# Kernel tuning notes

Hardware: AMD Instinct MI355X
Metric: run time of the kernel (lower is better)

## Reference

```python
import jax, jax.numpy as jnp
import numpy as np

ANGLE_SCALE = 100.0
DIST_SCALE = 100.0
DIST_BOUNDARY = 0.0
HID = 128
N_HIDDEN = 2  # output_layer
EPS = 1e-08


def _mlp(x, w0, b0, ws, bs):
    # Linear, then N_HIDDEN x (ReLU, Linear)
    h = x @ w0 + b0
    for i in range(ws.shape[0]):
        h = jax.nn.relu(h) @ ws[i] + bs[i]
    return h


def _capsule_endpoints(x):
    # x: [..., 9] -> A, B endpoints of capsule segment, radius r
    c, s = jnp.cos(x[..., 3:4] * ANGLE_SCALE), jnp.sin(x[..., 3:4] * ANGLE_SCALE)
    half = x[..., 2:3] / 2
    ctr = x[..., 0:2]
    off = jnp.concatenate([half * c, half * s], axis=-1)
    return ctr - off, ctr + off, x[..., 4:5]


def _pt_seg_dist(P, A, AB, AB_sq):
    t = jnp.clip(((P - A) * AB).sum(-1, keepdims=True) / AB_sq, 0.0, 1.0)
    Q = A + t * AB
    return jnp.linalg.norm(P - Q, axis=-1, keepdims=True)


def _dist_to_capsule(init_e, query_e):
    A1, B1, r1 = _capsule_endpoints(init_e)
    A2, B2, r2 = _capsule_endpoints(query_e)
    A1B1, A2B2 = B1 - A1, B2 - A2
    s1 = (A1B1 ** 2).sum(-1, keepdims=True) + EPS
    s2 = (A2B2 ** 2).sum(-1, keepdims=True) + EPS
    d = jnp.minimum(
        jnp.minimum(_pt_seg_dist(A2, A1, A1B1, s1), _pt_seg_dist(B2, A1, A1B1, s1)),
        jnp.minimum(_pt_seg_dist(A1, A2, A2B2, s2), _pt_seg_dist(B1, A2, A2B2, s2)),
    )
    return d - r1 - r2


def setup_inputs() -> dict:
    key = jax.random.key(0)
    ks = jax.random.split(key, 32)
    B, O, T = 64, 64, 64
    f = lambda k, shp, scale=1.0: jax.random.normal(k, shp, dtype=jnp.float32) * scale
    inp = {
        'init_x': f(ks[0], (B, O, 9)),
        'query_x': f(ks[1], (B, T, 9)),
        'init_v': f(ks[2], (B, O, 2)),
        'query_v': f(ks[3], (B, T, 2)),
        'init_angular_v': f(ks[4], (B, O, 1)),
        'query_angular_v': f(ks[5], (B, T, 1)),
        'trunk_w0': f(ks[6], (9, HID), 0.3), 'trunk_b0': f(ks[7], (HID,), 0.1),
        'trunk_ws': f(ks[8], (N_HIDDEN, HID, HID), 0.08), 'trunk_bs': f(ks[9], (N_HIDDEN, HID), 0.1),
        'branch_w0': f(ks[10], (5, HID), 0.3), 'branch_b0': f(ks[11], (HID,), 0.1),
        'branch_ws': f(ks[12], (N_HIDDEN, HID, HID), 0.08), 'branch_bs': f(ks[13], (N_HIDDEN, HID), 0.1),
        'out_w': f(ks[14], (HID, 3), 0.08), 'out_b': f(ks[15], (3,), 0.1),
        'spring_w0': f(ks[16], (1, HID), 0.3), 'spring_b0': f(ks[17], (HID,), 0.1),
        'spring_w1': f(ks[18], (HID, 1), 0.08), 'spring_b1': f(ks[19], (1,), 0.1),
        'joint_w0': f(ks[20], (15, HID), 0.3), 'joint_b0': f(ks[21], (HID,), 0.1),
        'joint_w1': f(ks[22], (HID, 2), 0.08), 'joint_b1': f(ks[23], (2,), 0.1),
    }
    return inp


def reference(init_x, query_x, init_v, query_v, init_angular_v, query_angular_v,
              trunk_w0, trunk_b0, trunk_ws, trunk_bs,
              branch_w0, branch_b0, branch_ws, branch_bs,
              out_w, out_b, spring_w0, spring_b0, spring_w1, spring_b1,
              joint_w0, joint_b0, joint_w1, joint_b1):
    B, O, _ = init_x.shape
    T = query_x.shape[1]
    # pairwise broadcast: init along obj axis (dim1), query along target axis (dim2)
    init_e = jnp.broadcast_to(init_x[:, :, None, :], (B, O, T, 9))
    query_e = jnp.broadcast_to(query_x[:, None, :, :], (B, O, T, 9))
    rel = query_e[..., :2] - init_e[..., :2]
    query_e = jnp.concatenate([rel, query_e[..., 2:]], axis=-1)
    init_e = jnp.concatenate([jnp.zeros_like(rel), init_e[..., 2:]], axis=-1)
    qv = query_v[:, None, :, :] - init_v[:, :, None, :]           # [B,O,T,2]
    qav = query_angular_v[:, None, :, :] - init_angular_v[:, :, None, :]  # [B,O,T,1]
    iav = jnp.broadcast_to(init_angular_v[:, :, None, :], (B, O, T, 1))

    dist = _dist_to_capsule(init_e, query_e)
    dist_mask = (dist <= DIST_BOUNDARY).astype(jnp.float32)
    dist_input = dist * dist_mask * DIST_SCALE

    branch_in = init_e[..., :5]
    trunk_in = jnp.concatenate([query_e[..., :5], qv, qav, dist_input], axis=-1)
    branch_out = _mlp(branch_in, branch_w0, branch_b0, branch_ws, branch_bs)
    trunk_out = _mlp(trunk_in, trunk_w0, trunk_b0, trunk_ws, trunk_bs)
    force = (branch_out * trunk_out) @ out_w + out_b  # [B,O,T,3]

    # spring force
    have_spring = ((init_e[..., 8:9] == query_e[..., 8:9]) & (init_e[..., 8:9] > 0)).astype(jnp.float32)
    dvec = init_e[..., :2] - query_e[..., :2]
    length = jnp.linalg.norm(dvec, axis=-1, keepdims=True)
    dvec = dvec / (length + EPS)
    sf = jax.nn.relu(length @ spring_w0 + spring_b0) @ spring_w1 + spring_b1  # [B,O,T,1]
    sf = sf * dvec
    sf = jnp.concatenate([sf, jnp.zeros_like(sf[..., :1])], axis=-1) * have_spring

    # joint force (torch .long() truncates toward zero)
    i7, q7 = init_e[..., 7:8], query_e[..., 7:8]
    have_joint = ((jnp.trunc(i7) == jnp.trunc(q7)) & (i7 > 0)).astype(jnp.float32)
    joint_in = jnp.concatenate([init_e[..., :5], query_e[..., :5], qv, iav, qav, i7 - jnp.trunc(i7)], axis=-1)
    jf = jax.nn.relu(joint_in @ joint_w0 + joint_b0) @ joint_w1 + joint_b1  # [B,O,T,2]
    jf = jf * have_joint
    jf = jnp.concatenate([jf, jnp.zeros_like(jf[..., :1])], axis=-1)

    force = force * dist_mask + sf + jf
    return force
```

## Files before the change

### kernel.cpp

```cpp
#include <hip/hip_runtime.h>
#include <math.h>


typedef _Float16 h4v __attribute__((ext_vector_type(4)));
typedef _Float16 h8v __attribute__((ext_vector_type(8)));
typedef float    f4v __attribute__((ext_vector_type(4)));

#define AH 136

#define TW0_OFF 0
#define JW0_OFF 4096
#define TWS_OFF 8192
#define BW0_OFF 40960
#define BWS_OFF 45056
#define W_TOTAL 77824
#define BR_OFF_F (W_TOTAL/2)

#define H_ACTA 0
#define H_ACTB 8704
#define H_TINB 8704
#define H_JINB 10752
#define SMH_SIZE 17408

#define F_SCAL  0
#define SMF_SIZE 384

#define FRAG_BLOCKS 304
#define BR_BLOCKS   256

__global__ __launch_bounds__(256)
void prep_kernel(const float* __restrict__ tw0, const float* __restrict__ tws,
                 const float* __restrict__ jw0, const float* __restrict__ bw0,
                 const float* __restrict__ bws, const float* __restrict__ bb0,
                 const float* __restrict__ bbs, const float* __restrict__ init_x,
                 _Float16* __restrict__ wsH, float* __restrict__ brw)
{
    __shared__ float bsm[2*16*132];
    const int tid = threadIdx.x;

    if (blockIdx.x < FRAG_BLOCKS) {
        int idx = blockIdx.x * 256 + tid;
        if (idx >= W_TOTAL) return;
        const int j = idx & 7;
        const int lane = (idx >> 3) & 63;
        const int q = lane >> 4, r = lane & 15;
        _Float16 v;
        if (idx < JW0_OFF) {
            int mt = idx >> 9;
            int k = q*8 + j, m = mt*16 + r;
            v = (k < 9) ? (_Float16)tw0[k*128 + m] : (_Float16)0.f;
        } else if (idx < TWS_OFF) {
            int mt = (idx - JW0_OFF) >> 9;
            int k = q*8 + j, m = mt*16 + r;
            v = (k < 15) ? (_Float16)jw0[k*128 + m] : (_Float16)0.f;
        } else if (idx < BW0_OFF) {
            int e = idx - TWS_OFF;
            int ks = (e >> 9) & 3, mt = (e >> 11) & 7, l = e >> 14;
            int k = ks*32 + q*8 + j, m = mt*16 + r;
            v = (_Float16)tws[l*16384 + k*128 + m];
        } else if (idx < BWS_OFF) {
            int mt = (idx - BW0_OFF) >> 9;
            int k = q*8 + j, m = mt*16 + r;
            v = (k < 5) ? (_Float16)bw0[k*128 + m] : (_Float16)0.f;
        } else {
            int e = idx - BWS_OFF;
            int ks = (e >> 9) & 3, mt = (e >> 11) & 7, l = e >> 14;
            int k = ks*32 + q*8 + j, m = mt*16 + r;
            v = (_Float16)bws[l*16384 + k*128 + m];
        }
        wsH[idx] = v;
        return;
    }

    const int blk2 = blockIdx.x - FRAG_BLOCKS;
    const int row0 = blk2*16;
    const int lane = tid & 63, w = tid >> 6;
    const int q = lane >> 4, r = lane & 15;
    float* h0 = bsm;
    float* h1 = bsm + 16*132;

    for (int e = tid; e < 2048; e += 256) {
        const int rw = e >> 7, n = e & 127;
        const float* ixp = init_x + (row0 + rw)*9;
        float acc = bb0[n];
        acc = fmaf(ixp[2], bw0[2*128 + n], acc);
        acc = fmaf(ixp[3], bw0[3*128 + n], acc);
        acc = fmaf(ixp[4], bw0[4*128 + n], acc);
        h0[rw*132 + n] = acc;
    }
    __syncthreads();

    #pragma unroll
    for (int L = 0; L < 2; ++L) {
        const float* Wg = bws + L*16384;
        const float* bi = bbs + L*128;
        const float* in = (L == 0) ? h0 : h1;
        #pragma unroll
        for (int mi = 0; mi < 2; ++mi) {
            const int mt = w + mi*4;
            const int m0 = mt*16 + q*4;
            h8v af[4];
            #pragma unroll
            for (int ks = 0; ks < 4; ++ks)
                #pragma unroll
                for (int j = 0; j < 8; ++j)
                    af[ks][j] = (_Float16)Wg[(ks*32 + q*8 + j)*128 + mt*16 + r];
            f4v acc = *(const f4v*)&bi[m0];
            #pragma unroll
            for (int ks = 0; ks < 4; ++ks) {
                f4v x0 = *(const f4v*)&in[r*132 + ks*32 + q*8];
                f4v x1 = *(const f4v*)&in[r*132 + ks*32 + q*8 + 4];
                h8v bf;
                #pragma unroll
                for (int i = 0; i < 4; ++i) {
                    bf[i]   = (_Float16)fmaxf(x0[i], 0.f);
                    bf[4+i] = (_Float16)fmaxf(x1[i], 0.f);
                }
                acc = __builtin_amdgcn_mfma_f32_16x16x32_f16(af[ks], bf, acc, 0, 0, 0);
            }
            if (L == 0)
                *(f4v*)&h1[r*132 + m0] = acc;
            else
                *(f4v*)&brw[(row0 + r)*128 + m0] = acc;
        }
        __syncthreads();
    }
}

__device__ __forceinline__ void layerK32_rw(const h8v af[2],
        const float* __restrict__ bias, const _Float16* __restrict__ inB,
        _Float16* __restrict__ actOut, int lane, int w)
{
    const int q = lane >> 4, r = lane & 15;
    #pragma unroll
    for (int nt = 0; nt < 4; ++nt) {
        h8v bf = *(const h8v*)&inB[(nt*64 + lane)*8];
        #pragma unroll
        for (int mi = 0; mi < 2; ++mi) {
            f4v acc = *(const f4v*)&bias[(2*w + mi)*16 + q*4];
            acc = __builtin_amdgcn_mfma_f32_16x16x32_f16(af[mi], bf, acc, 0, 0, 0);
            h4v o;
            #pragma unroll
            for (int i = 0; i < 4; ++i) o[i] = (_Float16)fmaxf(acc[i], 0.f);
            *(h4v*)&actOut[(nt*16 + r)*AH + (2*w + mi)*16 + q*4] = o;
        }
    }
}

__device__ __forceinline__ void layerK128_rw(const h8v af[2][4],
        const float* __restrict__ bias, const _Float16* __restrict__ actIn,
        _Float16* __restrict__ actOut, int lane, int w)
{
    const int q = lane >> 4, r = lane & 15;
    #pragma unroll
    for (int nt = 0; nt < 4; ++nt) {
        h8v bf[4];
        #pragma unroll
        for (int ks = 0; ks < 4; ++ks)
            bf[ks] = *(const h8v*)&actIn[(nt*16 + r)*AH + ks*32 + q*8];
        #pragma unroll
        for (int mi = 0; mi < 2; ++mi) {
            f4v acc = *(const f4v*)&bias[(2*w + mi)*16 + q*4];
            #pragma unroll
            for (int ks = 0; ks < 4; ++ks)
                acc = __builtin_amdgcn_mfma_f32_16x16x32_f16(af[mi][ks], bf[ks], acc, 0, 0, 0);
            h4v o;
            #pragma unroll
            for (int i = 0; i < 4; ++i) o[i] = (_Float16)fmaxf(acc[i], 0.f);
            *(h4v*)&actOut[(nt*16 + r)*AH + (2*w + mi)*16 + q*4] = o;
        }
    }
}

__device__ __forceinline__ void layerK128_regs_rw(const h8v af[2][4],
        const float* __restrict__ bias, const _Float16* __restrict__ actIn,
        f4v accT[2][4], int lane, int w)
{
    const int q = lane >> 4, r = lane & 15;
    #pragma unroll
    for (int nt = 0; nt < 4; ++nt) {
        h8v bf[4];
        #pragma unroll
        for (int ks = 0; ks < 4; ++ks)
            bf[ks] = *(const h8v*)&actIn[(nt*16 + r)*AH + ks*32 + q*8];
        #pragma unroll
        for (int mi = 0; mi < 2; ++mi) {
            f4v acc = *(const f4v*)&bias[(2*w + mi)*16 + q*4];
            #pragma unroll
            for (int ks = 0; ks < 4; ++ks)
                acc = __builtin_amdgcn_mfma_f32_16x16x32_f16(af[mi][ks], bf[ks], acc, 0, 0, 0);
            accT[mi][nt] = acc;
        }
    }
}

__global__ __launch_bounds__(256, 3)
void ff_kernel(const float* __restrict__ init_x,  const float* __restrict__ query_x,
               const float* __restrict__ init_v,  const float* __restrict__ query_v,
               const float* __restrict__ init_av, const float* __restrict__ query_av,
               const float* __restrict__ tb0, const float* __restrict__ tbs,
               const float* __restrict__ out_w, const float* __restrict__ out_b,
               const float* __restrict__ sw0, const float* __restrict__ sb0,
               const float* __restrict__ sw1, const float* __restrict__ sb1,
               const float* __restrict__ jb0,
               const float* __restrict__ jw1, const float* __restrict__ jb1,
               const _Float16* __restrict__ wsH, const float* __restrict__ brw,
               float* __restrict__ out)
{
    __shared__ __align__(16) _Float16 smh[SMH_SIZE];
    __shared__ float smf[SMF_SIZE];
    float* const fred = (float*)smh;
    const int tid = threadIdx.x;
    const int bid = blockIdx.x;
    const int o  = bid & 63;
    const int b  = bid >> 6;
    const int lane = tid & 63, w = tid >> 6;
    const int q = lane >> 4, r = lane & 15;
    const float* ix = init_x + (b*64 + o)*9;

    h8v afT0[2], afJ0[2], afT1[2][4], afT2[2][4];
    f4v br[2];
    #pragma unroll
    for (int mi = 0; mi < 2; ++mi) {
        const int mtg = 2*w + mi;
        afT0[mi] = *(const h8v*)&wsH[TW0_OFF + (mtg*64 + lane)*8];
        afJ0[mi] = *(const h8v*)&wsH[JW0_OFF + (mtg*64 + lane)*8];
        #pragma unroll
        for (int ks = 0; ks < 4; ++ks) {
            afT1[mi][ks] = *(const h8v*)&wsH[TWS_OFF + ((mtg*4 + ks)*64 + lane)*8];
            afT2[mi][ks] = *(const h8v*)&wsH[TWS_OFF + 16384 + ((mtg*4 + ks)*64 + lane)*8];
        }
        br[mi] = *(const f4v*)&brw[bid*128 + mtg*16 + q*4];
    }

    {
        const int tq = w*16 + r;
        const float* qx = query_x + (b*64 + tq)*9;
        const float ix0 = ix[0], ix1 = ix[1], ix2 = ix[2], ix3 = ix[3], ix4 = ix[4];
        const float ix7 = ix[7], ix8 = ix[8];
        const float qx0 = qx[0], qx1 = qx[1], qx2 = qx[2], qx3 = qx[3], qx4 = qx[4];
        const float qx7 = qx[7], qx8 = qx[8];
        const float rel0 = qx0 - ix0, rel1 = qx1 - ix1;

        float s1v, c1v; sincosf(ix3 * 100.f, &s1v, &c1v);
        float s2v, c2v; sincosf(qx3 * 100.f, &s2v, &c2v);
        const float h1 = ix2 * 0.5f, h2 = qx2 * 0.5f;
        const float o1x = h1*c1v, o1y = h1*s1v;
        const float o2x = h2*c2v, o2y = h2*s2v;
        const float A1x = -o1x, A1y = -o1y;
        const float A2x = rel0 - o2x, A2y = rel1 - o2y;
        const float B2x = rel0 + o2x, B2y = rel1 + o2y;
        const float ab1x = 2.f*o1x, ab1y = 2.f*o1y;
        const float ab2x = 2.f*o2x, ab2y = 2.f*o2y;
        const float s1sq = ab1x*ab1x + ab1y*ab1y + 1e-8f;
        const float s2sq = ab2x*ab2x + ab2y*ab2y + 1e-8f;

        float Px, Py, Ax, Ay, ABx, ABy, ss;
        if (q < 2) {
            Ax = A1x; Ay = A1y; ABx = ab1x; ABy = ab1y; ss = s1sq;
            Px = (q == 0) ? A2x : B2x;  Py = (q == 0) ? A2y : B2y;
        } else {
            Ax = A2x; Ay = A2y; ABx = ab2x; ABy = ab2y; ss = s2sq;
            Px = (q == 2) ? A1x : o1x;  Py = (q == 2) ? A1y : o1y;
        }
        float t = ((Px - Ax)*ABx + (Py - Ay)*ABy) / ss;
        t = fminf(fmaxf(t, 0.f), 1.f);
        const float dx = Px - (Ax + t*ABx);
        const float dy = Py - (Ay + t*ABy);
        float dq = sqrtf(dx*dx + dy*dy);
        dq = fminf(dq, __shfl_xor(dq, 16));
        dq = fminf(dq, __shfl_xor(dq, 32));

        if (q == 0) {
            const float dist = dq - ix4 - qx4;
            const float mask = (dist <= 0.f) ? 1.f : 0.f;
            const float dinp = dist * mask * 100.f;
            const float qv0 = query_v[(b*64+tq)*2+0] - init_v[(b*64+o)*2+0];
            const float qv1 = query_v[(b*64+tq)*2+1] - init_v[(b*64+o)*2+1];
            const float iav = init_av[b*64+o];
            const float qav = query_av[b*64+tq] - iav;

            const int fb = w*512 + r*8;
            h8v t0, t1 = {}, z = {};
            t0[0]=(_Float16)rel0; t0[1]=(_Float16)rel1; t0[2]=(_Float16)qx2;
            t0[3]=(_Float16)qx3;  t0[4]=(_Float16)qx4;  t0[5]=(_Float16)qv0;
            t0[6]=(_Float16)qv1;  t0[7]=(_Float16)qav;
            t1[0]=(_Float16)dinp;
            *(h8v*)&smh[H_TINB + fb]       = t0;
            *(h8v*)&smh[H_TINB + fb + 128] = t1;
            *(h8v*)&smh[H_TINB + fb + 256] = z;
            *(h8v*)&smh[H_TINB + fb + 384] = z;
            h8v j0, j1 = {};
            j0[0]=(_Float16)0.f;  j0[1]=(_Float16)0.f;  j0[2]=(_Float16)ix2;
            j0[3]=(_Float16)ix3;  j0[4]=(_Float16)ix4;  j0[5]=(_Float16)rel0;
            j0[6]=(_Float16)rel1; j0[7]=(_Float16)qx2;
            j1[0]=(_Float16)qx3;  j1[1]=(_Float16)qx4;  j1[2]=(_Float16)qv0;
            j1[3]=(_Float16)qv1;  j1[4]=(_Float16)iav;  j1[5]=(_Float16)qav;
            j1[6]=(_Float16)(ix7 - truncf(ix7));
            *(h8v*)&smh[H_JINB + fb]       = j0;
            *(h8v*)&smh[H_JINB + fb + 128] = j1;
            *(h8v*)&smh[H_JINB + fb + 256] = z;
            *(h8v*)&smh[H_JINB + fb + 384] = z;

            const float len = sqrtf(rel0*rel0 + rel1*rel1);
            const float inv = 1.f / (len + 1e-8f);
            smf[F_SCAL +       tq] = mask;
            smf[F_SCAL +  64 + tq] = len;
            smf[F_SCAL + 128 + tq] = -rel0 * inv;
            smf[F_SCAL + 192 + tq] = -rel1 * inv;
            smf[F_SCAL + 256 + tq] = ((ix8 == qx8) && (ix8 > 0.f)) ? 1.f : 0.f;
            smf[F_SCAL + 320 + tq] = ((truncf(ix7) == truncf(qx7)) && (ix7 > 0.f)) ? 1.f : 0.f;
        }
    }
    __syncthreads();

    float jf0[4] = {0,0,0,0}, jf1[4] = {0,0,0,0};
    layerK32_rw(afT0, tb0, smh + H_TINB, smh + H_ACTA, lane, w);
    {
        f4v bv[2], jwa[2], jwb[2];
        #pragma unroll
        for (int mi = 0; mi < 2; ++mi) {
            const int m0 = (2*w + mi)*16 + q*4;
            bv[mi]  = *(const f4v*)&jb0[m0];
            jwa[mi] = *(const f4v*)&jw1[m0*2];
            jwb[mi] = *(const f4v*)&jw1[m0*2 + 4];
        }
        #pragma unroll
        for (int nt = 0; nt < 4; ++nt) {
            h8v bf = *(const h8v*)&smh[H_JINB + (nt*64 + lane)*8];
            #pragma unroll
            for (int mi = 0; mi < 2; ++mi) {
                f4v a = bv[mi];
                a = __builtin_amdgcn_mfma_f32_16x16x32_f16(afJ0[mi], bf, a, 0, 0, 0);
                float jw[8] = {jwa[mi][0], jwa[mi][1], jwa[mi][2], jwa[mi][3],
                               jwb[mi][0], jwb[mi][1], jwb[mi][2], jwb[mi][3]};
                #pragma unroll
                for (int i = 0; i < 4; ++i) {
                    const float jh = fmaxf(a[i], 0.f);
                    jf0[nt] = fmaf(jh, jw[i*2+0], jf0[nt]);
                    jf1[nt] = fmaf(jh, jw[i*2+1], jf1[nt]);
                }
            }
        }
    }
    __syncthreads();

    layerK128_rw(afT1, tbs, smh + H_ACTA, smh + H_ACTB, lane, w);
    __syncthreads();

    f4v accT[2][4];
    layerK128_regs_rw(afT2, tbs + 128, smh + H_ACTB, accT, lane, w);

    float f0[4] = {0,0,0,0}, f1[4] = {0,0,0,0}, f2[4] = {0,0,0,0};
    float sp[4] = {0,0,0,0};

    #pragma unroll
    for (int mi = 0; mi < 2; ++mi) {
        const int m0 = (2*w + mi)*16 + q*4;
        f4v oa = *(const f4v*)&out_w[m0*3];
        f4v ob = *(const f4v*)&out_w[m0*3 + 4];
        f4v oc = *(const f4v*)&out_w[m0*3 + 8];
        float ow[12] = {oa[0],oa[1],oa[2],oa[3], ob[0],ob[1],ob[2],ob[3],
                        oc[0],oc[1],oc[2],oc[3]};
        #pragma unroll
        for (int nt = 0; nt < 4; ++nt)
            #pragma unroll
            for (int i = 0; i < 4; ++i) {
                const float prod = accT[mi][nt][i] * br[mi][i];
                f0[nt] = fmaf(prod, ow[i*3+0], f0[nt]);
                f1[nt] = fmaf(prod, ow[i*3+1], f1[nt]);
                f2[nt] = fmaf(prod, ow[i*3+2], f2[nt]);
            }
    }
    {
        float lenv[4];
        #pragma unroll
        for (int nt = 0; nt < 4; ++nt) lenv[nt] = smf[F_SCAL + 64 + nt*16 + r];
        #pragma unroll
        for (int mi = 0; mi < 2; ++mi) {
            const int m0 = (2*w + mi)*16 + q*4;
            f4v w0 = *(const f4v*)&sw0[m0];
            f4v b0 = *(const f4v*)&sb0[m0];
            f4v w1 = *(const f4v*)&sw1[m0];
            #pragma unroll
            for (int i = 0; i < 4; ++i)
                #pragma unroll
                for (int nt = 0; nt < 4; ++nt) {
                    const float sv = fmaxf(fmaf(lenv[nt], w0[i], b0[i]), 0.f);
                    sp[nt] = fmaf(sv, w1[i], sp[nt]);
                }
        }
    }
    #pragma unroll
    for (int nt = 0; nt < 4; ++nt) {
        float v[6] = {f0[nt], f1[nt], f2[nt], jf0[nt], jf1[nt], sp[nt]};
        #pragma unroll
        for (int k = 0; k < 6; ++k) {
            v[k] += __shfl_xor(v[k], 16);
            v[k] += __shfl_xor(v[k], 32);
        }
        if (lane < 16) {
            float* rd = &fred[((nt*16 + r)*4 + w)*7];
            rd[0]=v[0]; rd[1]=v[1]; rd[2]=v[2]; rd[3]=v[3]; rd[4]=v[4]; rd[5]=v[5];
        }
    }
    __syncthreads();

    if (tid < 64) {
        const int t = tid;
        float s0=0.f, s1=0.f, s2=0.f, s3=0.f, s4=0.f, s5=0.f;
        #pragma unroll
        for (int ww = 0; ww < 4; ++ww) {
            const float* rd = &fred[(t*4 + ww)*7];
            s0 += rd[0]; s1 += rd[1]; s2 += rd[2];
            s3 += rd[3]; s4 += rd[4]; s5 += rd[5];
        }
        const float mask = smf[F_SCAL + t];
        const float dvx  = smf[F_SCAL + 128 + t];
        const float dvy  = smf[F_SCAL + 192 + t];
        const float hs   = smf[F_SCAL + 256 + t];
        const float hj   = smf[F_SCAL + 320 + t];
        const float sf = (s5 + sb1[0]) * hs;
        const float j0 = (s3 + jb1[0]) * hj;
        const float j1 = (s4 + jb1[1]) * hj;
        float* op = out + (((b*64 + o)*64) + t)*3;
        op[0] = (s0 + out_b[0])*mask + sf*dvx + j0;
        op[1] = (s1 + out_b[1])*mask + sf*dvy + j1;
        op[2] = (s2 + out_b[2])*mask;
    }
}

extern "C" void kernel_launch(void* const* d_in, const int* in_sizes, int n_in,
                              void* d_out, int out_size, void* d_ws, size_t ws_size,
                              hipStream_t stream) {
    (void)in_sizes; (void)n_in; (void)out_size; (void)ws_size;
    _Float16* wsH = (_Float16*)d_ws;
    float* brw = (float*)d_ws + BR_OFF_F;

    prep_kernel<<<dim3(FRAG_BLOCKS + BR_BLOCKS), dim3(256), 0, stream>>>(
        (const float*)d_in[6],
        (const float*)d_in[8],
        (const float*)d_in[20],
        (const float*)d_in[10],
        (const float*)d_in[12],
        (const float*)d_in[11],
        (const float*)d_in[13],
        (const float*)d_in[0],
        wsH, brw);
    ff_kernel<<<dim3(64*64), dim3(256), 0, stream>>>(
        (const float*)d_in[0],  (const float*)d_in[1],  (const float*)d_in[2],
        (const float*)d_in[3],  (const float*)d_in[4],  (const float*)d_in[5],
        (const float*)d_in[7],  (const float*)d_in[9],
        (const float*)d_in[14], (const float*)d_in[15],
        (const float*)d_in[16], (const float*)d_in[17],
        (const float*)d_in[18], (const float*)d_in[19],
        (const float*)d_in[21],
        (const float*)d_in[22], (const float*)d_in[23],
        wsH, brw, (float*)d_out);
}
```

Baseline: 155.6 us.

## Run hidden layer in place in one LDS activation buffer to cut shared memory

Layer 1 of the trunk MLP now reads and writes a single activation buffer instead of ping-ponging between two. Each n-tile is loaded into registers, all threads synchronise, then results overwrite the same rows. This shrinks LDS per block so more blocks can be resident per CU. The cost is four extra block-wide barriers inside the layer loop. The reduction scratch moves into the input region and its indexing is changed to a per-wave layout.

Measured after the change: 161.2 us. 3.6% more time.

```diff
diff --git a/kernel.cpp b/kernel.cpp
--- a/kernel.cpp
+++ b/kernel.cpp
@@ -16,11 +16,10 @@
 #define W_TOTAL 77824
 #define BR_OFF_F (W_TOTAL/2)
 
-#define H_ACTA 0
-#define H_ACTB 8704
+#define H_ACT  0
 #define H_TINB 8704
 #define H_JINB 10752
-#define SMH_SIZE 17408
+#define SMH_SIZE 12800
 
 #define F_SCAL  0
 #define SMF_SIZE 384
@@ -147,31 +146,6 @@
     }
 }
 
-__device__ __forceinline__ void layerK128_rw(const h8v af[2][4],
-        const float* __restrict__ bias, const _Float16* __restrict__ actIn,
-        _Float16* __restrict__ actOut, int lane, int w)
-{
-    const int q = lane >> 4, r = lane & 15;
-    #pragma unroll
-    for (int nt = 0; nt < 4; ++nt) {
-        h8v bf[4];
-        #pragma unroll
-        for (int ks = 0; ks < 4; ++ks)
-            bf[ks] = *(const h8v*)&actIn[(nt*16 + r)*AH + ks*32 + q*8];
-        #pragma unroll
-        for (int mi = 0; mi < 2; ++mi) {
-            f4v acc = *(const f4v*)&bias[(2*w + mi)*16 + q*4];
-            #pragma unroll
-            for (int ks = 0; ks < 4; ++ks)
-                acc = __builtin_amdgcn_mfma_f32_16x16x32_f16(af[mi][ks], bf[ks], acc, 0, 0, 0);
-            h4v o;
-            #pragma unroll
-            for (int i = 0; i < 4; ++i) o[i] = (_Float16)fmaxf(acc[i], 0.f);
-            *(h4v*)&actOut[(nt*16 + r)*AH + (2*w + mi)*16 + q*4] = o;
-        }
-    }
-}
-
 __device__ __forceinline__ void layerK128_regs_rw(const h8v af[2][4],
         const float* __restrict__ bias, const _Float16* __restrict__ actIn,
         f4v accT[2][4], int lane, int w)
@@ -209,7 +183,7 @@
 {
     __shared__ __align__(16) _Float16 smh[SMH_SIZE];
     __shared__ float smf[SMF_SIZE];
-    float* const fred = (float*)smh;
+    float* const fred = (float*)(smh + H_TINB);
     const int tid = threadIdx.x;
     const int bid = blockIdx.x;
     const int o  = bid & 63;
@@ -315,7 +289,7 @@
     __syncthreads();
 
     float jf0[4] = {0,0,0,0}, jf1[4] = {0,0,0,0};
-    layerK32_rw(afT0, tb0, smh + H_TINB, smh + H_ACTA, lane, w);
+    layerK32_rw(afT0, tb0, smh + H_TINB, smh + H_ACT, lane, w);
     {
         f4v bv[2], jwa[2], jwb[2];
         #pragma unroll
@@ -345,11 +319,29 @@
     }
     __syncthreads();
 
-    layerK128_rw(afT1, tbs, smh + H_ACTA, smh + H_ACTB, lane, w);
+    #pragma unroll
+    for (int nt = 0; nt < 4; ++nt) {
+        h8v bf[4];
+        #pragma unroll
+        for (int ks = 0; ks < 4; ++ks)
+            bf[ks] = *(const h8v*)&smh[H_ACT + (nt*16 + r)*AH + ks*32 + q*8];
+        __syncthreads();
+        #pragma unroll
+        for (int mi = 0; mi < 2; ++mi) {
+            f4v acc = *(const f4v*)&tbs[(2*w + mi)*16 + q*4];
+            #pragma unroll
+            for (int ks = 0; ks < 4; ++ks)
+                acc = __builtin_amdgcn_mfma_f32_16x16x32_f16(afT1[mi][ks], bf[ks], acc, 0, 0, 0);
+            h4v oo;
+            #pragma unroll
+            for (int i = 0; i < 4; ++i) oo[i] = (_Float16)fmaxf(acc[i], 0.f);
+            *(h4v*)&smh[H_ACT + (nt*16 + r)*AH + (2*w + mi)*16 + q*4] = oo;
+        }
+    }
     __syncthreads();
 
     f4v accT[2][4];
-    layerK128_regs_rw(afT2, tbs + 128, smh + H_ACTB, accT, lane, w);
+    layerK128_regs_rw(afT2, tbs + 128, smh + H_ACT, accT, lane, w);
 
     float f0[4] = {0,0,0,0}, f1[4] = {0,0,0,0}, f2[4] = {0,0,0,0};
     float sp[4] = {0,0,0,0};
@@ -400,7 +392,7 @@
             v[k] += __shfl_xor(v[k], 32);
         }
         if (lane < 16) {
-            float* rd = &fred[((nt*16 + r)*4 + w)*7];
+            float* rd = &fred[w*448 + (nt*16 + r)*7];
             rd[0]=v[0]; rd[1]=v[1]; rd[2]=v[2]; rd[3]=v[3]; rd[4]=v[4]; rd[5]=v[5];
         }
     }
@@ -411,7 +403,7 @@
         float s0=0.f, s1=0.f, s2=0.f, s3=0.f, s4=0.f, s5=0.f;
         #pragma unroll
         for (int ww = 0; ww < 4; ++ww) {
-            const float* rd = &fred[(t*4 + ww)*7];
+            const float* rd = &fred[ww*448 + t*7];
             s0 += rd[0]; s1 += rd[1]; s2 += rd[2];
             s3 += rd[3]; s4 += rd[4]; s5 += rd[5];
         }
```

## Split last layer by query tile per wave, removing cross-wave reduction

Applied to the files above, without the earlier changes.

The last trunk layer, the joint MLP and the spring MLP are repartitioned. Each wave now owns 16 query rows and loops over all 8 hidden M-tiles, instead of owning 2 M-tiles for all 64 queries. This drops the shared-memory cross-wave reduction, its extra barrier and the smf scalar staging, and builds the joint B-operand in registers rather than in LDS. In exchange, layer-2 and joint weights are streamed from global memory inside the loop instead of being held in registers, which may add load latency.

Measured after the change: 184.5 us. +18.6%, slower.

```diff
diff --git a/kernel.cpp b/kernel.cpp
--- a/kernel.cpp
+++ b/kernel.cpp
@@ -18,12 +18,8 @@
 
 #define H_ACTA 0
 #define H_ACTB 8704
-#define H_TINB 8704
-#define H_JINB 10752
-#define SMH_SIZE 17408
-
-#define F_SCAL  0
-#define SMF_SIZE 384
+#define H_TINB 17408
+#define SMH_SIZE 19456
 
 #define FRAG_BLOCKS 304
 #define BR_BLOCKS   256
@@ -172,28 +168,6 @@
     }
 }
 
-__device__ __forceinline__ void layerK128_regs_rw(const h8v af[2][4],
-        const float* __restrict__ bias, const _Float16* __restrict__ actIn,
-        f4v accT[2][4], int lane, int w)
-{
-    const int q = lane >> 4, r = lane & 15;
-    #pragma unroll
-    for (int nt = 0; nt < 4; ++nt) {
-        h8v bf[4];
-        #pragma unroll
-        for (int ks = 0; ks < 4; ++ks)
-            bf[ks] = *(const h8v*)&actIn[(nt*16 + r)*AH + ks*32 + q*8];
-        #pragma unroll
-        for (int mi = 0; mi < 2; ++mi) {
-            f4v acc = *(const f4v*)&bias[(2*w + mi)*16 + q*4];
-            #pragma unroll
-            for (int ks = 0; ks < 4; ++ks)
-                acc = __builtin_amdgcn_mfma_f32_16x16x32_f16(af[mi][ks], bf[ks], acc, 0, 0, 0);
-            accT[mi][nt] = acc;
-        }
-    }
-}
-
 __global__ __launch_bounds__(256, 3)
 void ff_kernel(const float* __restrict__ init_x,  const float* __restrict__ query_x,
                const float* __restrict__ init_v,  const float* __restrict__ query_v,
@@ -208,8 +182,6 @@
                float* __restrict__ out)
 {
     __shared__ __align__(16) _Float16 smh[SMH_SIZE];
-    __shared__ float smf[SMF_SIZE];
-    float* const fred = (float*)smh;
     const int tid = threadIdx.x;
     const int bid = blockIdx.x;
     const int o  = bid & 63;
@@ -218,21 +190,18 @@
     const int q = lane >> 4, r = lane & 15;
     const float* ix = init_x + (b*64 + o)*9;
 
-    h8v afT0[2], afJ0[2], afT1[2][4], afT2[2][4];
-    f4v br[2];
+    h8v afT0[2], afT1[2][4];
     #pragma unroll
     for (int mi = 0; mi < 2; ++mi) {
         const int mtg = 2*w + mi;
         afT0[mi] = *(const h8v*)&wsH[TW0_OFF + (mtg*64 + lane)*8];
-        afJ0[mi] = *(const h8v*)&wsH[JW0_OFF + (mtg*64 + lane)*8];
-        #pragma unroll
-        for (int ks = 0; ks < 4; ++ks) {
+        #pragma unroll
+        for (int ks = 0; ks < 4; ++ks)
             afT1[mi][ks] = *(const h8v*)&wsH[TWS_OFF + ((mtg*4 + ks)*64 + lane)*8];
-            afT2[mi][ks] = *(const h8v*)&wsH[TWS_OFF + 16384 + ((mtg*4 + ks)*64 + lane)*8];
-        }
-        br[mi] = *(const f4v*)&brw[bid*128 + mtg*16 + q*4];
-    }
-
+    }
+
+    float maskS, dvxS, dvyS, hsS, hjS, lenS;
+    h8v bT, bJ;
     {
         const int tq = w*16 + r;
         const float* qx = query_x + (b*64 + tq)*9;
@@ -271,15 +240,44 @@
         dq = fminf(dq, __shfl_xor(dq, 16));
         dq = fminf(dq, __shfl_xor(dq, 32));
 
+        const float dist = dq - ix4 - qx4;
+        const float mask = (dist <= 0.f) ? 1.f : 0.f;
+        const float dinp = dist * mask * 100.f;
+        const float qv0 = query_v[(b*64+tq)*2+0] - init_v[(b*64+o)*2+0];
+        const float qv1 = query_v[(b*64+tq)*2+1] - init_v[(b*64+o)*2+1];
+        const float iav = init_av[b*64+o];
+        const float qav = query_av[b*64+tq] - iav;
+        const float len = sqrtf(rel0*rel0 + rel1*rel1);
+        const float inv = 1.f / (len + 1e-8f);
+        const float i7t = truncf(ix7);
+        const float fr7 = ix7 - i7t;
+
+        maskS = mask;
+        dvxS  = -rel0 * inv;
+        dvyS  = -rel1 * inv;
+        hsS   = ((ix8 == qx8) && (ix8 > 0.f)) ? 1.f : 0.f;
+        hjS   = ((i7t == truncf(qx7)) && (ix7 > 0.f)) ? 1.f : 0.f;
+        lenS  = len;
+
+        const bool g0 = (q == 0), g1 = (q == 1);
+        bT[0] = (_Float16)(g0 ? rel0 : g1 ? dinp : 0.f);
+        bT[1] = (_Float16)(g0 ? rel1 : 0.f);
+        bT[2] = (_Float16)(g0 ? qx2  : 0.f);
+        bT[3] = (_Float16)(g0 ? qx3  : 0.f);
+        bT[4] = (_Float16)(g0 ? qx4  : 0.f);
+        bT[5] = (_Float16)(g0 ? qv0  : 0.f);
+        bT[6] = (_Float16)(g0 ? qv1  : 0.f);
+        bT[7] = (_Float16)(g0 ? qav  : 0.f);
+        bJ[0] = (_Float16)(g1 ? qx3  : 0.f);
+        bJ[1] = (_Float16)(g1 ? qx4  : 0.f);
+        bJ[2] = (_Float16)(g0 ? ix2  : g1 ? qv0 : 0.f);
+        bJ[3] = (_Float16)(g0 ? ix3  : g1 ? qv1 : 0.f);
+        bJ[4] = (_Float16)(g0 ? ix4  : g1 ? iav : 0.f);
+        bJ[5] = (_Float16)(g0 ? rel0 : g1 ? qav : 0.f);
+        bJ[6] = (_Float16)(g0 ? rel1 : g1 ? fr7 : 0.f);
+        bJ[7] = (_Float16)(g0 ? qx2  : 0.f);
+
         if (q == 0) {
-            const float dist = dq - ix4 - qx4;
-            const float mask = (dist <= 0.f) ? 1.f : 0.f;
-            const float dinp = dist * mask * 100.f;
-            const float qv0 = query_v[(b*64+tq)*2+0] - init_v[(b*64+o)*2+0];
-            const float qv1 = query_v[(b*64+tq)*2+1] - init_v[(b*64+o)*2+1];
-            const float iav = init_av[b*64+o];
-            const float qav = query_av[b*64+tq] - iav;
-
             const int fb = w*512 + r*8;
             h8v t0, t1 = {}, z = {};
             t0[0]=(_Float16)rel0; t0[1]=(_Float16)rel1; t0[2]=(_Float16)qx2;
@@ -290,143 +288,73 @@
             *(h8v*)&smh[H_TINB + fb + 128] = t1;
             *(h8v*)&smh[H_TINB + fb + 256] = z;
             *(h8v*)&smh[H_TINB + fb + 384] = z;
-            h8v j0, j1 = {};
-            j0[0]=(_Float16)0.f;  j0[1]=(_Float16)0.f;  j0[2]=(_Float16)ix2;
-            j0[3]=(_Float16)ix3;  j0[4]=(_Float16)ix4;  j0[5]=(_Float16)rel0;
-            j0[6]=(_Float16)rel1; j0[7]=(_Float16)qx2;
-            j1[0]=(_Float16)qx3;  j1[1]=(_Float16)qx4;  j1[2]=(_Float16)qv0;
-            j1[3]=(_Float16)qv1;  j1[4]=(_Float16)iav;  j1[5]=(_Float16)qav;
-            j1[6]=(_Float16)(ix7 - truncf(ix7));
-            *(h8v*)&smh[H_JINB + fb]       = j0;
-            *(h8v*)&smh[H_JINB + fb + 128] = j1;
-            *(h8v*)&smh[H_JINB + fb + 256] = z;
-            *(h8v*)&smh[H_JINB + fb + 384] = z;
-
-            const float len = sqrtf(rel0*rel0 + rel1*rel1);
-            const float inv = 1.f / (len + 1e-8f);
-            smf[F_SCAL +       tq] = mask;
-            smf[F_SCAL +  64 + tq] = len;
-            smf[F_SCAL + 128 + tq] = -rel0 * inv;
-            smf[F_SCAL + 192 + tq] = -rel1 * inv;
-            smf[F_SCAL + 256 + tq] = ((ix8 == qx8) && (ix8 > 0.f)) ? 1.f : 0.f;
-            smf[F_SCAL + 320 + tq] = ((truncf(ix7) == truncf(qx7)) && (ix7 > 0.f)) ? 1.f : 0.f;
         }
     }
     __syncthreads();
 
-    float jf0[4] = {0,0,0,0}, jf1[4] = {0,0,0,0};
     layerK32_rw(afT0, tb0, smh + H_TINB, smh + H_ACTA, lane, w);
-    {
-        f4v bv[2], jwa[2], jwb[2];
-        #pragma unroll
-        for (int mi = 0; mi < 2; ++mi) {
-            const int m0 = (2*w + mi)*16 + q*4;
-            bv[mi]  = *(const f4v*)&jb0[m0];
-            jwa[mi] = *(const f4v*)&jw1[m0*2];
-            jwb[mi] = *(const f4v*)&jw1[m0*2 + 4];
-        }
-        #pragma unroll
-        for (int nt = 0; nt < 4; ++nt) {
-            h8v bf = *(const h8v*)&smh[H_JINB + (nt*64 + lane)*8];
-            #pragma unroll
-            for (int mi = 0; mi < 2; ++mi) {
-                f4v a = bv[mi];
-                a = __builtin_amdgcn_mfma_f32_16x16x32_f16(afJ0[mi], bf, a, 0, 0, 0);
-                float jw[8] = {jwa[mi][0], jwa[mi][1], jwa[mi][2], jwa[mi][3],
-                               jwb[mi][0], jwb[mi][1], jwb[mi][2], jwb[mi][3]};
-                #pragma unroll
-                for (int i = 0; i < 4; ++i) {
-                    const float jh = fmaxf(a[i], 0.f);
-                    jf0[nt] = fmaf(jh, jw[i*2+0], jf0[nt]);
-                    jf1[nt] = fmaf(jh, jw[i*2+1], jf1[nt]);
-                }
-            }
-        }
-    }
     __syncthreads();
 
     layerK128_rw(afT1, tbs, smh + H_ACTA, smh + H_ACTB, lane, w);
     __syncthreads();
 
-    f4v accT[2][4];
-    layerK128_regs_rw(afT2, tbs + 128, smh + H_ACTB, accT, lane, w);
-
-    float f0[4] = {0,0,0,0}, f1[4] = {0,0,0,0}, f2[4] = {0,0,0,0};
-    float sp[4] = {0,0,0,0};
-
-    #pragma unroll
-    for (int mi = 0; mi < 2; ++mi) {
-        const int m0 = (2*w + mi)*16 + q*4;
+    h8v bf[4];
+    #pragma unroll
+    for (int ks = 0; ks < 4; ++ks)
+        bf[ks] = *(const h8v*)&smh[H_ACTB + (w*16 + r)*AH + ks*32 + q*8];
+
+    float jf0 = 0.f, jf1 = 0.f, f0 = 0.f, f1 = 0.f, f2 = 0.f, sp = 0.f;
+    #pragma unroll 2
+    for (int mt = 0; mt < 8; ++mt) {
+        const int m0 = mt*16 + q*4;
+        h8v aJ = *(const h8v*)&wsH[JW0_OFF + (mt*64 + lane)*8];
+        f4v accJ = *(const f4v*)&jb0[m0];
+        accJ = __builtin_amdgcn_mfma_f32_16x16x32_f16(aJ, bJ, accJ, 0, 0, 0);
+        f4v jwa = *(const f4v*)&jw1[m0*2];
+        f4v jwb = *(const f4v*)&jw1[m0*2 + 4];
+        {
+            const float h0r = fmaxf(accJ[0], 0.f), h1r = fmaxf(accJ[1], 0.f);
+            const float h2r = fmaxf(accJ[2], 0.f), h3r = fmaxf(accJ[3], 0.f);
+            jf0 = fmaf(h0r, jwa[0], fmaf(h1r, jwa[2], fmaf(h2r, jwb[0], fmaf(h3r, jwb[2], jf0))));
+            jf1 = fmaf(h0r, jwa[1], fmaf(h1r, jwa[3], fmaf(h2r, jwb[1], fmaf(h3r, jwb[3], jf1))));
+        }
+        f4v acc = *(const f4v*)&tbs[128 + m0];
+        #pragma unroll
+        for (int ks = 0; ks < 4; ++ks) {
+            h8v a2 = *(const h8v*)&wsH[TWS_OFF + 16384 + ((mt*4 + ks)*64 + lane)*8];
+            acc = __builtin_amdgcn_mfma_f32_16x16x32_f16(a2, bf[ks], acc, 0, 0, 0);
+        }
+        f4v brv = *(const f4v*)&brw[bid*128 + m0];
         f4v oa = *(const f4v*)&out_w[m0*3];
         f4v ob = *(const f4v*)&out_w[m0*3 + 4];
         f4v oc = *(const f4v*)&out_w[m0*3 + 8];
-        float ow[12] = {oa[0],oa[1],oa[2],oa[3], ob[0],ob[1],ob[2],ob[3],
-                        oc[0],oc[1],oc[2],oc[3]};
-        #pragma unroll
-        for (int nt = 0; nt < 4; ++nt)
-            #pragma unroll
-            for (int i = 0; i < 4; ++i) {
-                const float prod = accT[mi][nt][i] * br[mi][i];
-                f0[nt] = fmaf(prod, ow[i*3+0], f0[nt]);
-                f1[nt] = fmaf(prod, ow[i*3+1], f1[nt]);
-                f2[nt] = fmaf(prod, ow[i*3+2], f2[nt]);
-            }
-    }
-    {
-        float lenv[4];
-        #pragma unroll
-        for (int nt = 0; nt < 4; ++nt) lenv[nt] = smf[F_SCAL + 64 + nt*16 + r];
-        #pragma unroll
-        for (int mi = 0; mi < 2; ++mi) {
-            const int m0 = (2*w + mi)*16 + q*4;
-            f4v w0 = *(const f4v*)&sw0[m0];
-            f4v b0 = *(const f4v*)&sb0[m0];
-            f4v w1 = *(const f4v*)&sw1[m0];
-            #pragma unroll
-            for (int i = 0; i < 4; ++i)
-                #pragma unroll
-                for (int nt = 0; nt < 4; ++nt) {
-                    const float sv = fmaxf(fmaf(lenv[nt], w0[i], b0[i]), 0.f);
-                    sp[nt] = fmaf(sv, w1[i], sp[nt]);
-                }
-        }
-    }
-    #pragma unroll
-    for (int nt = 0; nt < 4; ++nt) {
-        float v[6] = {f0[nt], f1[nt], f2[nt], jf0[nt], jf1[nt], sp[nt]};
-        #pragma unroll
-        for (int k = 0; k < 6; ++k) {
-            v[k] += __shfl_xor(v[k], 16);
-            v[k] += __shfl_xor(v[k], 32);
-        }
-        if (lane < 16) {
-            float* rd = &fred[((nt*16 + r)*4 + w)*7];
-            rd[0]=v[0]; rd[1]=v[1]; rd[2]=v[2]; rd[3]=v[3]; rd[4]=v[4]; rd[5]=v[5];
-        }
-    }
-    __syncthreads();
-
-    if (tid < 64) {
-        const int t = tid;
-        float s0=0.f, s1=0.f, s2=0.f, s3=0.f, s4=0.f, s5=0.f;
-        #pragma unroll
-        for (int ww = 0; ww < 4; ++ww) {
-            const float* rd = &fred[(t*4 + ww)*7];
-            s0 += rd[0]; s1 += rd[1]; s2 += rd[2];
-            s3 += rd[3]; s4 += rd[4]; s5 += rd[5];
-        }
-        const float mask = smf[F_SCAL + t];
-        const float dvx  = smf[F_SCAL + 128 + t];
-        const float dvy  = smf[F_SCAL + 192 + t];
-        const float hs   = smf[F_SCAL + 256 + t];
-        const float hj   = smf[F_SCAL + 320 + t];
-        const float sf = (s5 + sb1[0]) * hs;
-        const float j0 = (s3 + jb1[0]) * hj;
-        const float j1 = (s4 + jb1[1]) * hj;
-        float* op = out + (((b*64 + o)*64) + t)*3;
-        op[0] = (s0 + out_b[0])*mask + sf*dvx + j0;
-        op[1] = (s1 + out_b[1])*mask + sf*dvy + j1;
-        op[2] = (s2 + out_b[2])*mask;
+        const float p0 = acc[0]*brv[0], p1 = acc[1]*brv[1];
+        const float p2 = acc[2]*brv[2], p3 = acc[3]*brv[3];
+        f0 += p0*oa[0] + p1*oa[3] + p2*ob[2] + p3*oc[1];
+        f1 += p0*oa[1] + p1*ob[0] + p2*ob[3] + p3*oc[2];
+        f2 += p0*oa[2] + p1*ob[1] + p2*oc[0] + p3*oc[3];
+        f4v w0v = *(const f4v*)&sw0[m0];
+        f4v b0v = *(const f4v*)&sb0[m0];
+        f4v w1v = *(const f4v*)&sw1[m0];
+        #pragma unroll
+        for (int i = 0; i < 4; ++i)
+            sp = fmaf(fmaxf(fmaf(lenS, w0v[i], b0v[i]), 0.f), w1v[i], sp);
+    }
+
+    f0  += __shfl_xor(f0, 16);  f0  += __shfl_xor(f0, 32);
+    f1  += __shfl_xor(f1, 16);  f1  += __shfl_xor(f1, 32);
+    f2  += __shfl_xor(f2, 16);  f2  += __shfl_xor(f2, 32);
+    jf0 += __shfl_xor(jf0, 16); jf0 += __shfl_xor(jf0, 32);
+    jf1 += __shfl_xor(jf1, 16); jf1 += __shfl_xor(jf1, 32);
+    sp  += __shfl_xor(sp, 16);  sp  += __shfl_xor(sp, 32);
+    if (q == 0) {
+        const float sf = (sp + sb1[0]) * hsS;
+        const float j0 = (jf0 + jb1[0]) * hjS;
+        const float j1 = (jf1 + jb1[1]) * hjS;
+        float* op = out + ((bid*64) + w*16 + r)*3;
+        op[0] = (f0 + out_b[0])*maskS + sf*dvxS + j0;
+        op[1] = (f1 + out_b[1])*maskS + sf*dvyS + j1;
+        op[2] = (f2 + out_b[2])*maskS;
     }
 }
 
```
